# Kernel tuning notes

Hardware: AMD Instinct MI355X
Metric: run time of the kernel (lower is better)

## Reference

```python
import jax, jax.numpy as jnp
import numpy as np

B, T, D = 16, 2048, 64


def setup_inputs() -> dict:
    key = jax.random.key(0)
    kq, kk, kv, kb = jax.random.split(key, 4)
    q = jax.random.normal(kq, (B, T, D), dtype=jnp.float32)
    k = jax.random.normal(kk, (B, T, D), dtype=jnp.float32)
    v = jax.random.normal(kv, (B, T, D), dtype=jnp.float32)
    add_attn = jax.random.normal(kb, (B, T, T), dtype=jnp.float32)
    return {"q": q, "k": k, "v": v, "add_attn": add_attn}


def reference(q, k, v, add_attn):
    # scale = 1/sqrt(head_dim), the standard value passed by callers
    scale = 1.0 / jnp.sqrt(jnp.asarray(q.shape[-1], dtype=q.dtype))
    # [B, T, T] attention logits: bmm(q, k^T) * scale + additive bias
    attn = jnp.einsum('btd,bsd->bts', q, k) * scale + add_attn
    # softmax over keys (dim=2); dropout p=0.0 is identity
    attn = jax.nn.softmax(attn, axis=2)
    # [B, T, D] weighted values
    output = jnp.einsum('bts,bsd->btd', attn, v)
    return (output, attn)
```

## Files before the change

kernel.cpp:

```cpp
#include <hip/hip_runtime.h>
#include <stdint.h>

#define NB 16
#define NT 2048
#define ND 64

typedef __attribute__((ext_vector_type(8))) short bf16x8;
typedef __attribute__((ext_vector_type(4))) float f32x4;
typedef __attribute__((ext_vector_type(4))) _Float16 f16x4;

__device__ __forceinline__ unsigned short f2bf(float f) {
    union { float f; unsigned u; } v; v.f = f;
    unsigned r = v.u + 0x7fffu + ((v.u >> 16) & 1u);
    return (unsigned short)(r >> 16);
}
__device__ __forceinline__ unsigned short f2h(float f) {
    union { _Float16 h; unsigned short u; } v; v.h = (_Float16)f; return v.u;
}

__global__ __launch_bounds__(256) void prep_k(const float* __restrict__ Q,
                                              const float* __restrict__ K,
                                              const float* __restrict__ V,
                                              unsigned short* __restrict__ qbf,
                                              unsigned short* __restrict__ kbf,
                                              unsigned short* __restrict__ vt)
{
    const size_t i = (size_t)blockIdx.x * 256 + threadIdx.x;
    const int which = blockIdx.y;
    if (which == 2) {
        float4 v4 = ((const float4*)V)[i];
        const int d4 = (int)(i & 15);
        const int t  = (int)((i >> 4) & (NT - 1));
        const int b  = (int)(i >> 15);
        unsigned short* base = vt + ((size_t)b * ND + d4 * 4) * NT + t;
        base[0]      = f2h(v4.x);
        base[NT]     = f2h(v4.y);
        base[2 * NT] = f2h(v4.z);
        base[3 * NT] = f2h(v4.w);
    } else {
        const float4* src = (which == 0) ? (const float4*)Q : (const float4*)K;
        unsigned short* dst = (which == 0) ? qbf : kbf;
        float4 v4 = src[i];
        union { unsigned short s[4]; unsigned long long ll; } u;
        u.s[0] = f2bf(v4.x); u.s[1] = f2bf(v4.y);
        u.s[2] = f2bf(v4.z); u.s[3] = f2bf(v4.w);
        *(unsigned long long*)(dst + 4 * i) = u.ll;
    }
}

__global__ __launch_bounds__(256, 2)
void attn_onepass(const unsigned short* __restrict__ qbf,
                  const unsigned short* __restrict__ kbf,
                  const unsigned short* __restrict__ vt,
                  const float* __restrict__ Bias,
                  float* __restrict__ Out,
                  float* __restrict__ Attn)
{
    const int b = blockIdx.y, q0 = blockIdx.x * 16;
    const int tid = threadIdx.x, w = tid >> 6, lane = tid & 63;
    const int n = lane & 15, qd = lane >> 4;
    const int kw0 = w * 512;

    __shared__ float s_rs[4][16];
    __shared__ float s_o[4 * 16 * 68];

    const unsigned short* qp = qbf + ((size_t)(b * NT + q0 + n)) * ND + qd * 8;
    const bf16x8 qf0 = *(const bf16x8*)qp;
    const bf16x8 qf1 = *(const bf16x8*)(qp + 32);
    const float* Bb = Bias + ((size_t)b * NT + q0 + n) * NT;
    float* Ab = Attn + ((size_t)b * NT + q0 + n) * NT;
    const unsigned short* vtb = vt + (size_t)b * ND * NT + (size_t)n * NT;

    f16x4 ev[32];
    bf16x8 kb0[6], kb1[6];
    float4 bb[8];
#pragma unroll
    for (int i = 0; i < 6; ++i) {
        const unsigned short* kp = kbf + ((size_t)(b * NT + kw0 + 16 * i + n)) * ND + qd * 8;
        kb0[i] = *(const bf16x8*)kp;
        kb1[i] = *(const bf16x8*)(kp + 32);
    }
#pragma unroll
    for (int i = 0; i < 8; ++i)
        bb[i] = *(const float4*)(Bb + kw0 + 16 * i + qd * 4);

    float rs = 0.f;
#pragma unroll
    for (int t = 0; t < 32; ++t) {
        const bf16x8 kf0 = kb0[t % 6];
        const bf16x8 kf1 = kb1[t % 6];
        const float4 bs = bb[t & 7];
        if (t + 6 < 32) {
            const unsigned short* kp =
                kbf + ((size_t)(b * NT + kw0 + 16 * (t + 6) + n)) * ND + qd * 8;
            kb0[t % 6] = *(const bf16x8*)kp;
            kb1[t % 6] = *(const bf16x8*)(kp + 32);
        }
        if (t + 8 < 32)
            bb[t & 7] = *(const float4*)(Bb + kw0 + 16 * (t + 8) + qd * 4);
        f32x4 acc = {0.f, 0.f, 0.f, 0.f};
        acc = __builtin_amdgcn_mfma_f32_16x16x32_bf16(kf0, qf0, acc, 0, 0, 0);
        acc = __builtin_amdgcn_mfma_f32_16x16x32_bf16(kf1, qf1, acc, 0, 0, 0);
        float e0 = __expf(__builtin_fmaf(acc[0], 0.125f, bs.x - 2.0f));
        float e1 = __expf(__builtin_fmaf(acc[1], 0.125f, bs.y - 2.0f));
        float e2 = __expf(__builtin_fmaf(acc[2], 0.125f, bs.z - 2.0f));
        float e3 = __expf(__builtin_fmaf(acc[3], 0.125f, bs.w - 2.0f));
        union { _Float16 h[4]; f16x4 v; } u;
        u.h[0] = (_Float16)e0; u.h[1] = (_Float16)e1;
        u.h[2] = (_Float16)e2; u.h[3] = (_Float16)e3;
        ev[t] = u.v;
        rs += (e0 + e1) + (e2 + e3);
    }

    f16x4 vr0[3][4], vr1[3][4];
#pragma unroll
    for (int i = 0; i < 3; ++i)
#pragma unroll
        for (int dt = 0; dt < 4; ++dt) {
            const unsigned short* vp = vtb + kw0 + 32 * i + qd * 4 + (size_t)dt * 16 * NT;
            vr0[i][dt] = *(const f16x4*)(const void*)vp;
            vr1[i][dt] = *(const f16x4*)(const void*)(vp + 16);
        }

    rs += __shfl_xor(rs, 16, 64);
    rs += __shfl_xor(rs, 32, 64);
    if (lane < 16) s_rs[w][lane] = rs;
    __syncthreads();
    const float tot = (s_rs[0][n] + s_rs[1][n]) + (s_rs[2][n] + s_rs[3][n]);
    const float inv = 1.0f / tot;

    f32x4 oacc[4];
#pragma unroll
    for (int dt = 0; dt < 4; ++dt) oacc[dt] = (f32x4){0.f, 0.f, 0.f, 0.f};

#pragma unroll
    for (int tp = 0; tp < 16; ++tp) {
        const int key0 = kw0 + 32 * tp;
        f16x4 va0[4], va1[4];
#pragma unroll
        for (int dt = 0; dt < 4; ++dt) { va0[dt] = vr0[tp % 3][dt]; va1[dt] = vr1[tp % 3][dt]; }
        if (tp + 3 < 16) {
#pragma unroll
            for (int dt = 0; dt < 4; ++dt) {
                const unsigned short* vp =
                    vtb + kw0 + 32 * (tp + 3) + qd * 4 + (size_t)dt * 16 * NT;
                vr0[tp % 3][dt] = *(const f16x4*)(const void*)vp;
                vr1[tp % 3][dt] = *(const f16x4*)(const void*)(vp + 16);
            }
        }
        const f16x4 e0v = ev[2 * tp];
        const f16x4 e1v = ev[2 * tp + 1];
        float4 s0, s1;
        s0.x = (float)e0v[0] * inv; s0.y = (float)e0v[1] * inv;
        s0.z = (float)e0v[2] * inv; s0.w = (float)e0v[3] * inv;
        s1.x = (float)e1v[0] * inv; s1.y = (float)e1v[1] * inv;
        s1.z = (float)e1v[2] * inv; s1.w = (float)e1v[3] * inv;
        *(float4*)(Ab + key0 + qd * 4) = s0;
        *(float4*)(Ab + key0 + 16 + qd * 4) = s1;
#pragma unroll
        for (int dt = 0; dt < 4; ++dt) {
            oacc[dt] = __builtin_amdgcn_mfma_f32_16x16x16f16(va0[dt], e0v, oacc[dt], 0, 0, 0);
            oacc[dt] = __builtin_amdgcn_mfma_f32_16x16x16f16(va1[dt], e1v, oacc[dt], 0, 0, 0);
        }
    }

#pragma unroll
    for (int dt = 0; dt < 4; ++dt) {
        float4 t4;
        t4.x = oacc[dt][0] * inv; t4.y = oacc[dt][1] * inv;
        t4.z = oacc[dt][2] * inv; t4.w = oacc[dt][3] * inv;
        *(float4*)&s_o[(w * 16 + n) * 68 + dt * 16 + qd * 4] = t4;
    }
    __syncthreads();
    {
        const int row = tid >> 4, d4 = (tid & 15) * 4;
        float4 o0 = *(const float4*)&s_o[(0 * 16 + row) * 68 + d4];
        float4 o1 = *(const float4*)&s_o[(1 * 16 + row) * 68 + d4];
        float4 o2 = *(const float4*)&s_o[(2 * 16 + row) * 68 + d4];
        float4 o3 = *(const float4*)&s_o[(3 * 16 + row) * 68 + d4];
        float4 o;
        o.x = (o0.x + o1.x) + (o2.x + o3.x);
        o.y = (o0.y + o1.y) + (o2.y + o3.y);
        o.z = (o0.z + o1.z) + (o2.z + o3.z);
        o.w = (o0.w + o1.w) + (o2.w + o3.w);
        *(float4*)(Out + ((size_t)b * NT + q0 + row) * ND + d4) = o;
    }
}

__device__ __forceinline__ bf16x8 pack8(float4 a, float4 b) {
    union { unsigned short s[8]; bf16x8 v; } u;
    u.s[0] = f2bf(a.x); u.s[1] = f2bf(a.y); u.s[2] = f2bf(a.z); u.s[3] = f2bf(a.w);
    u.s[4] = f2bf(b.x); u.s[5] = f2bf(b.y); u.s[6] = f2bf(b.z); u.s[7] = f2bf(b.w);
    return u.v;
}
__global__ __launch_bounds__(256, 2)
void attn_fused(const float* __restrict__ Q, const float* __restrict__ K,
                const float* __restrict__ V, const float* __restrict__ Bias,
                float* __restrict__ Out, float* __restrict__ Attn)
{
    const int b  = blockIdx.y;
    const int q0 = blockIdx.x * 16;
    const int tid  = threadIdx.x;
    const int w    = tid >> 6;
    const int lane = tid & 63;
    const int n  = lane & 15;
    const int qd = lane >> 4;
    const int kw0 = w * 512;
    __shared__ float s_rs[4][16];
    __shared__ __align__(16) unsigned char s_rp[4][16 * 80];
    const float* Qb = Q + ((size_t)b * NT + q0) * ND;
    const float* Kb = K + (size_t)b * NT * ND;
    const float* Vb = V + (size_t)b * NT * ND;
    const float* Bb = Bias + ((size_t)b * NT + q0) * NT;
    float* Ab = Attn + ((size_t)b * NT + q0) * NT;
    float* Ob = Out  + ((size_t)b * NT + q0) * ND;
    bf16x8 qf0, qf1;
    {
        const float* qp = Qb + n * ND + qd * 8;
        qf0 = pack8(*(const float4*)qp,        *(const float4*)(qp + 4));
        qf1 = pack8(*(const float4*)(qp + 32), *(const float4*)(qp + 36));
    }
    float ev[32][4];
    float rs = 0.f;
#pragma unroll
    for (int t = 0; t < 32; ++t) {
        const int key0 = kw0 + 16 * t;
        const float* kp = Kb + (size_t)(key0 + n) * ND + qd * 8;
        bf16x8 kf0 = pack8(*(const float4*)kp,        *(const float4*)(kp + 4));
        bf16x8 kf1 = pack8(*(const float4*)(kp + 32), *(const float4*)(kp + 36));
        f32x4 acc = {0.f, 0.f, 0.f, 0.f};
        acc = __builtin_amdgcn_mfma_f32_16x16x32_bf16(kf0, qf0, acc, 0, 0, 0);
        acc = __builtin_amdgcn_mfma_f32_16x16x32_bf16(kf1, qf1, acc, 0, 0, 0);
        float4 bs = *(const float4*)(Bb + (size_t)n * NT + key0 + qd * 4);
        float e0 = __expf(acc[0] * 0.125f + bs.x);
        float e1 = __expf(acc[1] * 0.125f + bs.y);
        float e2 = __expf(acc[2] * 0.125f + bs.z);
        float e3 = __expf(acc[3] * 0.125f + bs.w);
        ev[t][0] = e0; ev[t][1] = e1; ev[t][2] = e2; ev[t][3] = e3;
        rs += (e0 + e1) + (e2 + e3);
    }
    rs += __shfl_xor(rs, 16, 64);
    rs += __shfl_xor(rs, 32, 64);
    if (lane < 16) s_rs[w][lane] = rs;
    __syncthreads();
    const float tot = (s_rs[0][n] + s_rs[1][n]) + (s_rs[2][n] + s_rs[3][n]);
    const float inv = 1.0f / tot;
    f32x4 oacc[4];
#pragma unroll
    for (int dt = 0; dt < 4; ++dt) oacc[dt] = (f32x4){0.f, 0.f, 0.f, 0.f};
    unsigned char* rp = &s_rp[w][0];
#pragma unroll
    for (int c = 0; c < 16; ++c) {
        const int kbase = kw0 + 32 * c;
#pragma unroll
        for (int tt = 0; tt < 2; ++tt) {
            const int t = 2 * c + tt;
            float p0 = ev[t][0] * inv;
            float p1 = ev[t][1] * inv;
            float p2 = ev[t][2] * inv;
            float p3 = ev[t][3] * inv;
            float4 pv; pv.x = p0; pv.y = p1; pv.z = p2; pv.w = p3;
            *(float4*)(Ab + (size_t)n * NT + kbase + 16 * tt + qd * 4) = pv;
            union { unsigned short s[4]; unsigned long long ll; } pu;
            pu.s[0] = f2bf(p0); pu.s[1] = f2bf(p1);
            pu.s[2] = f2bf(p2); pu.s[3] = f2bf(p3);
            *(unsigned long long*)(rp + n * 80 + (16 * tt + 4 * qd) * 2) = pu.ll;
        }
        __syncthreads();
        bf16x8 pf;
        {
            union { uint4 u; bf16x8 v; } uu;
            uu.u = *(const uint4*)(rp + n * 80 + qd * 16);
            pf = uu.v;
        }
#pragma unroll
        for (int dt = 0; dt < 4; ++dt) {
            const int d = dt * 16 + n;
            const float* vp = Vb + (size_t)(kbase + qd * 8) * ND + d;
            float4 va, vb4;
            va.x  = vp[0];   va.y  = vp[64];  va.z  = vp[128]; va.w  = vp[192];
            vb4.x = vp[256]; vb4.y = vp[320]; vb4.z = vp[384]; vb4.w = vp[448];
            bf16x8 vf = pack8(va, vb4);
            oacc[dt] = __builtin_amdgcn_mfma_f32_16x16x32_bf16(vf, pf, oacc[dt], 0, 0, 0);
        }
        __syncthreads();
    }
#pragma unroll
    for (int dt = 0; dt < 4; ++dt)
#pragma unroll
        for (int r = 0; r < 4; ++r)
            atomicAdd(Ob + (size_t)n * ND + dt * 16 + qd * 4 + r, oacc[dt][r]);
}

extern "C" void kernel_launch(void* const* d_in, const int* in_sizes, int n_in,
                              void* d_out, int out_size, void* d_ws, size_t ws_size,
                              hipStream_t stream)
{
    const float* q    = (const float*)d_in[0];
    const float* k    = (const float*)d_in[1];
    const float* v    = (const float*)d_in[2];
    const float* bias = (const float*)d_in[3];
    float* out  = (float*)d_out;
    float* attn = out + (size_t)NB * NT * ND;

    const size_t elems = (size_t)NB * NT * ND;
    const size_t need  = 3 * elems * 2;

    if (ws_size >= need) {
        unsigned short* qbf = (unsigned short*)d_ws;
        unsigned short* kbf = qbf + elems;
        unsigned short* vtb = kbf + elems;
        prep_k<<<dim3((unsigned)(elems / 4 / 256), 3), 256, 0, stream>>>(q, k, v, qbf, kbf, vtb);
        attn_onepass<<<dim3(NT / 16, NB), 256, 0, stream>>>(qbf, kbf, vtb, bias, out, attn);
    } else {
        hipMemsetAsync(out, 0, (size_t)NB * NT * ND * sizeof(float), stream);
        dim3 grid(NT / 16, NB);
        attn_fused<<<grid, 256, 0, stream>>>(q, k, v, bias, out, attn);
    }
}
```

Before: 262.4 us.

## Stage bias loads and attn stores through swizzled LDS for coalesced row access

Bias tiles are now loaded with row-contiguous coalesced float4 reads into a per-wave swizzled LDS buffer, double-buffered across four key groups. Attention probabilities are written to LDS and then flushed as contiguous 512-byte row segments instead of the scattered MFMA-layout stores. The block index is remapped to interleave batches and query tiles, and sched_barriers pin the placement of loads. This targets inefficient global access on the large bias read and attn write. In exchange it adds 64KB of LDS per block, which may lower occupancy, plus extra LDS traffic and fewer registers held for K prefetch.

```diff
diff --git a/kernel.cpp b/kernel.cpp
--- a/kernel.cpp
+++ b/kernel.cpp
@@ -56,61 +56,95 @@
                   float* __restrict__ Out,
                   float* __restrict__ Attn)
 {
-    const int b = blockIdx.y, q0 = blockIdx.x * 16;
+    const int flat = blockIdx.x + (NT / 16) * blockIdx.y;
+    const int lin  = (flat & 7) * 256 + (flat >> 3);
+    const int b    = lin >> 7;
+    const int q0   = (lin & 127) * 16;
+
     const int tid = threadIdx.x, w = tid >> 6, lane = tid & 63;
     const int n = lane & 15, qd = lane >> 4;
     const int kw0 = w * 512;
-
+    const int Lr = lane >> 5;
+    const int Lc = lane & 31;
+
+    __shared__ float pool[4 * 4096];
     __shared__ float s_rs[4][16];
-    __shared__ float s_o[4 * 16 * 68];
+    float* bw = pool + w * 4096;
+
+    const int swz_rd = (qd * 4) ^ ((n & 3) << 2);
 
     const unsigned short* qp = qbf + ((size_t)(b * NT + q0 + n)) * ND + qd * 8;
     const bf16x8 qf0 = *(const bf16x8*)qp;
     const bf16x8 qf1 = *(const bf16x8*)(qp + 32);
-    const float* Bb = Bias + ((size_t)b * NT + q0 + n) * NT;
-    float* Ab = Attn + ((size_t)b * NT + q0 + n) * NT;
+    const float* BiasBase = Bias + ((size_t)b * NT + q0) * NT;
     const unsigned short* vtb = vt + (size_t)b * ND * NT + (size_t)n * NT;
+    const unsigned short* kbp = kbf + ((size_t)(b * NT + kw0 + n)) * ND + qd * 8;
 
     f16x4 ev[32];
-    bf16x8 kb0[6], kb1[6];
-    float4 bb[8];
-#pragma unroll
-    for (int i = 0; i < 6; ++i) {
-        const unsigned short* kp = kbf + ((size_t)(b * NT + kw0 + 16 * i + n)) * ND + qd * 8;
+    bf16x8 kb0[4], kb1[4];
+    float4 fr[8];
+
+#pragma unroll
+    for (int i = 0; i < 4; ++i) {
+        const unsigned short* kp = kbp + (size_t)(16 * i) * ND;
         kb0[i] = *(const bf16x8*)kp;
         kb1[i] = *(const bf16x8*)(kp + 32);
     }
-#pragma unroll
-    for (int i = 0; i < 8; ++i)
-        bb[i] = *(const float4*)(Bb + kw0 + 16 * i + qd * 4);
+
+#define BIAS_LD(g)                                                            \
+    _Pragma("unroll")                                                         \
+    for (int j = 0; j < 8; ++j)                                               \
+        fr[j] = *(const float4*)(BiasBase + (size_t)(2 * j + Lr) * NT +       \
+                                 kw0 + 128 * (g) + 4 * Lc);
+
+#define BIAS_ST(g)                                                            \
+    _Pragma("unroll")                                                         \
+    for (int j = 0; j < 8; ++j) {                                             \
+        const int row = 2 * j + Lr;                                           \
+        *(float4*)&bw[((g) & 1) * 2048 + (Lc >> 2) * 256 + row * 16 +         \
+                      ((4 * (Lc & 3)) ^ ((row & 3) << 2))] = fr[j];           \
+    }
+
+#define PH1_GROUP(g)                                                          \
+    _Pragma("unroll")                                                         \
+    for (int tt = 0; tt < 8; ++tt) {                                          \
+        const int t = (g) * 8 + tt;                                           \
+        const bf16x8 kf0 = kb0[t & 3];                                        \
+        const bf16x8 kf1 = kb1[t & 3];                                        \
+        const float4 bs =                                                     \
+            *(const float4*)&bw[((g) & 1) * 2048 + tt * 256 + n * 16 + swz_rd];\
+        f32x4 acc = {0.f, 0.f, 0.f, 0.f};                                     \
+        acc = __builtin_amdgcn_mfma_f32_16x16x32_bf16(kf0, qf0, acc, 0, 0, 0);\
+        acc = __builtin_amdgcn_mfma_f32_16x16x32_bf16(kf1, qf1, acc, 0, 0, 0);\
+        float e0 = __expf(__builtin_fmaf(acc[0], 0.125f, bs.x - 2.0f));       \
+        float e1 = __expf(__builtin_fmaf(acc[1], 0.125f, bs.y - 2.0f));       \
+        float e2 = __expf(__builtin_fmaf(acc[2], 0.125f, bs.z - 2.0f));       \
+        float e3 = __expf(__builtin_fmaf(acc[3], 0.125f, bs.w - 2.0f));       \
+        union { _Float16 h[4]; f16x4 v; } u;                                  \
+        u.h[0] = (_Float16)e0; u.h[1] = (_Float16)e1;                         \
+        u.h[2] = (_Float16)e2; u.h[3] = (_Float16)e3;                         \
+        ev[t] = u.v;                                                          \
+        rs += (e0 + e1) + (e2 + e3);                                          \
+        if (t + 4 < 32) {                                                     \
+            const unsigned short* kp = kbp + (size_t)(16 * (t + 4)) * ND;     \
+            kb0[t & 3] = *(const bf16x8*)kp;                                  \
+            kb1[t & 3] = *(const bf16x8*)(kp + 32);                           \
+        }                                                                     \
+    }
 
     float rs = 0.f;
-#pragma unroll
-    for (int t = 0; t < 32; ++t) {
-        const bf16x8 kf0 = kb0[t % 6];
-        const bf16x8 kf1 = kb1[t % 6];
-        const float4 bs = bb[t & 7];
-        if (t + 6 < 32) {
-            const unsigned short* kp =
-                kbf + ((size_t)(b * NT + kw0 + 16 * (t + 6) + n)) * ND + qd * 8;
-            kb0[t % 6] = *(const bf16x8*)kp;
-            kb1[t % 6] = *(const bf16x8*)(kp + 32);
-        }
-        if (t + 8 < 32)
-            bb[t & 7] = *(const float4*)(Bb + kw0 + 16 * (t + 8) + qd * 4);
-        f32x4 acc = {0.f, 0.f, 0.f, 0.f};
-        acc = __builtin_amdgcn_mfma_f32_16x16x32_bf16(kf0, qf0, acc, 0, 0, 0);
-        acc = __builtin_amdgcn_mfma_f32_16x16x32_bf16(kf1, qf1, acc, 0, 0, 0);
-        float e0 = __expf(__builtin_fmaf(acc[0], 0.125f, bs.x - 2.0f));
-        float e1 = __expf(__builtin_fmaf(acc[1], 0.125f, bs.y - 2.0f));
-        float e2 = __expf(__builtin_fmaf(acc[2], 0.125f, bs.z - 2.0f));
-        float e3 = __expf(__builtin_fmaf(acc[3], 0.125f, bs.w - 2.0f));
-        union { _Float16 h[4]; f16x4 v; } u;
-        u.h[0] = (_Float16)e0; u.h[1] = (_Float16)e1;
-        u.h[2] = (_Float16)e2; u.h[3] = (_Float16)e3;
-        ev[t] = u.v;
-        rs += (e0 + e1) + (e2 + e3);
-    }
+    BIAS_LD(0)
+    BIAS_ST(0)
+    BIAS_LD(1) __builtin_amdgcn_sched_barrier(0);
+    PH1_GROUP(0)
+    BIAS_ST(1)
+    BIAS_LD(2) __builtin_amdgcn_sched_barrier(0);
+    PH1_GROUP(1)
+    BIAS_ST(2)
+    BIAS_LD(3) __builtin_amdgcn_sched_barrier(0);
+    PH1_GROUP(2)
+    BIAS_ST(3)
+    PH1_GROUP(3)
 
     f16x4 vr0[3][4], vr1[3][4];
 #pragma unroll
@@ -121,6 +155,7 @@
             vr0[i][dt] = *(const f16x4*)(const void*)vp;
             vr1[i][dt] = *(const f16x4*)(const void*)(vp + 16);
         }
+    __builtin_amdgcn_sched_barrier(0);
 
     rs += __shfl_xor(rs, 16, 64);
     rs += __shfl_xor(rs, 32, 64);
@@ -135,19 +170,6 @@
 
 #pragma unroll
     for (int tp = 0; tp < 16; ++tp) {
-        const int key0 = kw0 + 32 * tp;
-        f16x4 va0[4], va1[4];
-#pragma unroll
-        for (int dt = 0; dt < 4; ++dt) { va0[dt] = vr0[tp % 3][dt]; va1[dt] = vr1[tp % 3][dt]; }
-        if (tp + 3 < 16) {
-#pragma unroll
-            for (int dt = 0; dt < 4; ++dt) {
-                const unsigned short* vp =
-                    vtb + kw0 + 32 * (tp + 3) + qd * 4 + (size_t)dt * 16 * NT;
-                vr0[tp % 3][dt] = *(const f16x4*)(const void*)vp;
-                vr1[tp % 3][dt] = *(const f16x4*)(const void*)(vp + 16);
-            }
-        }
         const f16x4 e0v = ev[2 * tp];
         const f16x4 e1v = ev[2 * tp + 1];
         float4 s0, s1;
@@ -155,15 +177,42 @@
         s0.z = (float)e0v[2] * inv; s0.w = (float)e0v[3] * inv;
         s1.x = (float)e1v[0] * inv; s1.y = (float)e1v[1] * inv;
         s1.z = (float)e1v[2] * inv; s1.w = (float)e1v[3] * inv;
-        *(float4*)(Ab + key0 + qd * 4) = s0;
-        *(float4*)(Ab + key0 + 16 + qd * 4) = s1;
+        {
+            const int sa = (2 * (tp & 3)) * 256 + n * 16 + swz_rd;
+            *(float4*)&bw[sa] = s0;
+            *(float4*)&bw[sa + 256] = s1;
+        }
 #pragma unroll
         for (int dt = 0; dt < 4; ++dt) {
-            oacc[dt] = __builtin_amdgcn_mfma_f32_16x16x16f16(va0[dt], e0v, oacc[dt], 0, 0, 0);
-            oacc[dt] = __builtin_amdgcn_mfma_f32_16x16x16f16(va1[dt], e1v, oacc[dt], 0, 0, 0);
-        }
-    }
-
+            oacc[dt] = __builtin_amdgcn_mfma_f32_16x16x16f16(vr0[tp % 3][dt], e0v, oacc[dt], 0, 0, 0);
+            oacc[dt] = __builtin_amdgcn_mfma_f32_16x16x16f16(vr1[tp % 3][dt], e1v, oacc[dt], 0, 0, 0);
+        }
+        __builtin_amdgcn_sched_barrier(0);
+        if (tp + 3 < 16) {
+#pragma unroll
+            for (int dt = 0; dt < 4; ++dt) {
+                const unsigned short* vp =
+                    vtb + kw0 + 32 * (tp + 3) + qd * 4 + (size_t)dt * 16 * NT;
+                vr0[tp % 3][dt] = *(const f16x4*)(const void*)vp;
+                vr1[tp % 3][dt] = *(const f16x4*)(const void*)(vp + 16);
+            }
+        }
+        __builtin_amdgcn_sched_barrier(0);
+        if ((tp & 3) == 3) {
+            const int F = tp >> 2;
+#pragma unroll
+            for (int j = 0; j < 8; ++j) {
+                const int rr = 2 * j + Lr;
+                float4 vfl = *(const float4*)&bw[(Lc >> 2) * 256 + rr * 16 +
+                                                 ((4 * (Lc & 3)) ^ ((rr & 3) << 2))];
+                *(float4*)(Attn + ((size_t)(b * NT + q0 + rr)) * NT +
+                           kw0 + 128 * F + 4 * Lc) = vfl;
+            }
+        }
+    }
+
+    __syncthreads();
+    float* s_o = pool;
 #pragma unroll
     for (int dt = 0; dt < 4; ++dt) {
         float4 t4;
```

New measurement: 294.4 us. 1.12x slower.
